# Kernel tuning notes

Measured on AMD Instinct MI355X. Metric: run time of the kernel, lower is better.

## Reference

```python
import jax, jax.numpy as jnp
import numpy as np
from jax import lax

H = 64  # hidden_size

def _lstm_layer(x, w_ih, w_hh, b_ih, b_hh):
    # x: (B, T, in). PyTorch gate order [i, f, g, o]; gates = x@W_ih^T + h@W_hh^T + b_ih + b_hh.
    B, T, _ = x.shape
    xw = jnp.einsum('bti,gi->btg', x, w_ih) + (b_ih + b_hh)  # (B, T, 4H), input projection hoisted out of scan

    def step(carry, xw_t):
        h, c = carry
        gates = xw_t + h @ w_hh.T                     # (B, 4H)
        i, f, g, o = jnp.split(gates, 4, axis=-1)
        i = jax.nn.sigmoid(i)
        f = jax.nn.sigmoid(f)
        g = jnp.tanh(g)
        o = jax.nn.sigmoid(o)
        c = f * c + i * g
        h = o * jnp.tanh(c)
        return (h, c), h

    h0 = jnp.zeros((B, H), dtype=x.dtype)
    c0 = jnp.zeros((B, H), dtype=x.dtype)
    (h_n, _), hs = lax.scan(step, (h0, c0), jnp.swapaxes(xw, 0, 1))  # hs: (T, B, H)
    return jnp.swapaxes(hs, 0, 1), h_n


def setup_inputs() -> dict:
    key = jax.random.key(0)
    ks = jax.random.split(key, 12)
    s = 1.0 / np.sqrt(H)  # PyTorch LSTM init scale
    return {
        'x':     jax.random.normal(ks[0], (2048, 512, 4), dtype=jnp.float32),
        'w_ih0': jax.random.uniform(ks[1], (4 * H, 4), jnp.float32, -s, s),
        'w_hh0': jax.random.uniform(ks[2], (4 * H, H), jnp.float32, -s, s),
        'b_ih0': jax.random.uniform(ks[3], (4 * H,), jnp.float32, -s, s),
        'b_hh0': jax.random.uniform(ks[4], (4 * H,), jnp.float32, -s, s),
        'w_ih1': jax.random.uniform(ks[5], (4 * H, H), jnp.float32, -s, s),
        'w_hh1': jax.random.uniform(ks[6], (4 * H, H), jnp.float32, -s, s),
        'b_ih1': jax.random.uniform(ks[7], (4 * H,), jnp.float32, -s, s),
        'b_hh1': jax.random.uniform(ks[8], (4 * H,), jnp.float32, -s, s),
        'fc_w':  jax.random.uniform(ks[9], (H, H), jnp.float32, -s, s),
        'fc_b':  jax.random.uniform(ks[10], (H,), jnp.float32, -s, s),
    }


def reference(x, w_ih0, w_hh0, b_ih0, b_hh0, w_ih1, w_hh1, b_ih1, b_hh1, fc_w, fc_b):
    # 2-layer LSTM (eval mode: inter-layer dropout inactive), take last layer's final hidden,
    # then Linear + tanh.
    h1_seq, _ = _lstm_layer(x, w_ih0, w_hh0, b_ih0, b_hh0)
    _, h_n = _lstm_layer(h1_seq, w_ih1, w_hh1, b_ih1, b_hh1)
    return jnp.tanh(h_n @ fc_w.T + fc_b)
```

## Files before the change

kernel.cpp:

```cpp
#include <hip/hip_runtime.h>


#define HID 64
#define TSTEPS 512
#define MB 8
#define BLK 256
#define HSTR 88
#define LOG2E  1.4426950408889634f
#define LOG2E2 2.8853900817779268f

typedef _Float16 f16;
typedef _Float16 half8 __attribute__((ext_vector_type(8)));
typedef _Float16 half4 __attribute__((ext_vector_type(4)));
typedef float f32x4 __attribute__((ext_vector_type(4)));

__device__ __forceinline__ float tanh2(float y) {
    return fmaf(2.0f, __builtin_amdgcn_rcpf(1.0f + __builtin_amdgcn_exp2f(-y)), -1.0f);
}

__global__ __launch_bounds__(BLK, 1) void lstm_mfma(
    const float* __restrict__ x,
    const float* __restrict__ w_ih0,
    const float* __restrict__ w_hh0,
    const float* __restrict__ b_ih0,
    const float* __restrict__ b_hh0,
    const float* __restrict__ w_ih1,
    const float* __restrict__ w_hh1,
    const float* __restrict__ b_ih1,
    const float* __restrict__ b_hh1,
    const float* __restrict__ fc_w,
    const float* __restrict__ fc_b,
    float* __restrict__ out)
{
    __shared__ f16 xs[TSTEPS * MB * 4];
    __shared__ f16 h0s[4][MB * HSTR];
    __shared__ f16 h1s[2][MB * HSTR];

    const int tid  = threadIdx.x;
    const int wl   = tid >> 6;
    const int l    = tid & 63;
    const int quad = l >> 4;
    const int l15  = l & 15;
    const int b0   = blockIdx.x * MB;

    const int RM = (l15 < 8) ? l15 : ((l15 & 4) | ((l15 + 2) & 3));

    for (int it = tid; it < MB * TSTEPS; it += BLK) {
        const int m = it >> 9;
        const int t = it & 511;
        const float4 v = *((const float4*)x + (size_t)(b0 + m) * TSTEPS + t);
        *(half4*)(xs + (t * MB + m) * 4) =
            (half4){ (f16)v.x, (f16)v.y, (f16)v.z, (f16)v.w };
    }
    for (int it = tid; it < MB * HSTR; it += BLK) {
        h0s[0][it] = (f16)0.f; h0s[1][it] = (f16)0.f;
        h0s[2][it] = (f16)0.f; h0s[3][it] = (f16)0.f;
        h1s[0][it] = (f16)0.f; h1s[1][it] = (f16)0.f;
    }

    half8 B0[4][3];
    half8 B1[4][4];
    f32x4 bias0[4], bias1[4];
    const half8 Z = { (f16)0.f,(f16)0.f,(f16)0.f,(f16)0.f,
                      (f16)0.f,(f16)0.f,(f16)0.f,(f16)0.f };
    #pragma unroll
    for (int ti = 0; ti < 4; ++ti) {
        const int n = (wl + 4 * ti) * 16 + l15;
        const float sc = (ti == 2) ? LOG2E2 : LOG2E;
        {
            const float bval = (b_ih0[n] + b_hh0[n]) * sc;
            half8 pz = Z;
            if (quad == 0) {
                const float4 v = *(const float4*)(w_ih0 + n * 4);
                pz[0] = (f16)(v.x * sc); pz[1] = (f16)(v.y * sc);
                pz[2] = (f16)(v.z * sc); pz[3] = (f16)(v.w * sc);
            }
            B0[ti][0] = pz;
            #pragma unroll
            for (int ks = 0; ks < 2; ++ks) {
                const int ko = ks * 32 + quad * 8;
                const float4 a = *(const float4*)(w_hh0 + n * HID + ko);
                const float4 b = *(const float4*)(w_hh0 + n * HID + ko + 4);
                B0[ti][1 + ks] = (half8){
                    (f16)(a.x*sc),(f16)(a.y*sc),(f16)(a.z*sc),(f16)(a.w*sc),
                    (f16)(b.x*sc),(f16)(b.y*sc),(f16)(b.z*sc),(f16)(b.w*sc) };
            }
            bias0[ti] = (f32x4){ bval, bval, bval, bval };
        }
        {
            const float bval = (b_ih1[n] + b_hh1[n]) * sc;
            #pragma unroll
            for (int ks = 0; ks < 2; ++ks) {
                const int ko = ks * 32 + quad * 8;
                const float4 a = *(const float4*)(w_ih1 + n * HID + ko);
                const float4 b = *(const float4*)(w_ih1 + n * HID + ko + 4);
                B1[ti][ks] = (half8){
                    (f16)(a.x*sc),(f16)(a.y*sc),(f16)(a.z*sc),(f16)(a.w*sc),
                    (f16)(b.x*sc),(f16)(b.y*sc),(f16)(b.z*sc),(f16)(b.w*sc) };
                const float4 c = *(const float4*)(w_hh1 + n * HID + ko);
                const float4 d = *(const float4*)(w_hh1 + n * HID + ko + 4);
                B1[ti][2 + ks] = (half8){
                    (f16)(c.x*sc),(f16)(c.y*sc),(f16)(c.z*sc),(f16)(c.w*sc),
                    (f16)(d.x*sc),(f16)(d.y*sc),(f16)(d.z*sc),(f16)(d.w*sc) };
            }
            bias1[ti] = (f32x4){ bval, bval, bval, bval };
        }
    }

    const int  mrow = (quad & 1) * 4 + (quad & 2);
    const int  uu   = wl * 16 + l15;
    const int  hb   = RM * HSTR + quad * 8;
    float c00 = 0.f, c01 = 0.f;
    float c10 = 0.f, c11 = 0.f;
    f32x4 g0[4], g1[4];

    auto load_x = [&](int r) -> half4 {
        return *(const half4*)(xs + (r * MB + RM) * 4);
    };
    auto l0_mfma = [&](half4 xv, half8 A1, half8 A2) {
        half8 ax = Z;
        if (quad == 0) { ax[0]=xv[0]; ax[1]=xv[1]; ax[2]=xv[2]; ax[3]=xv[3]; }
        #pragma unroll
        for (int ti = 0; ti < 4; ++ti) {
            f32x4 acc;
            acc    = __builtin_amdgcn_mfma_f32_16x16x32_f16(ax, B0[ti][0], bias0[ti], 0, 0, 0);
            acc    = __builtin_amdgcn_mfma_f32_16x16x32_f16(A1, B0[ti][1], acc, 0, 0, 0);
            g0[ti] = __builtin_amdgcn_mfma_f32_16x16x32_f16(A2, B0[ti][2], acc, 0, 0, 0);
        }
    };
    auto l1_mfma = [&](half8 A1, half8 A2, half8 A3, half8 A4) {
        #pragma unroll
        for (int ti = 0; ti < 4; ++ti) {
            f32x4 acc;
            acc    = __builtin_amdgcn_mfma_f32_16x16x32_f16(A1, B1[ti][0], bias1[ti], 0, 0, 0);
            acc    = __builtin_amdgcn_mfma_f32_16x16x32_f16(A2, B1[ti][1], acc, 0, 0, 0);
            acc    = __builtin_amdgcn_mfma_f32_16x16x32_f16(A3, B1[ti][2], acc, 0, 0, 0);
            g1[ti] = __builtin_amdgcn_mfma_f32_16x16x32_f16(A4, B1[ti][3], acc, 0, 0, 0);
        }
    };
    auto act_store = [&](const f32x4* gg, f16* dst, float& ca, float& cb) {
        #pragma unroll
        for (int j = 0; j < 2; ++j) {
            const float ei = __builtin_amdgcn_exp2f(-gg[0][j]);
            const float ef = __builtin_amdgcn_exp2f(-gg[1][j]);
            const float eg = __builtin_amdgcn_exp2f(-gg[2][j]);
            const float eo = __builtin_amdgcn_exp2f(-gg[3][j]);
            float& c = j ? cb : ca;
            const float af = 1.0f + ef;
            const float P  = (1.0f + ei) * (1.0f + eg);
            const float N  = fmaf(c * P, 1.0f, (1.0f - eg) * af);
            c = N * __builtin_amdgcn_rcpf(P * af);
            const float ym = fminf(-LOG2E2 * c, 126.0f);
            const float ec = __builtin_amdgcn_exp2f(ym);
            const float r2 = __builtin_amdgcn_rcpf((1.0f + eo) * (1.0f + ec));
            dst[(mrow + j) * HSTR + uu] = (f16)((1.0f - ec) * r2);
        }
    };

    __syncthreads();

    half4 xv = load_x(0);

    #pragma unroll 1
    for (int r = 0; r < TSTEPS; ++r) {
        const f16* h0rd = h0s[(r + 3) & 3];
        const half8 A1 = *(const half8*)(h0rd + hb);
        const half8 A2 = *(const half8*)(h0rd + hb + 32);
        if (r >= 2) act_store(g1, h1s[r & 1], c10, c11);
        l0_mfma(xv, A1, A2);
        __syncthreads();
        const f16* h1rd = h1s[r & 1];
        const half8 A3 = *(const half8*)(h1rd + hb);
        const half8 A4 = *(const half8*)(h1rd + hb + 32);
        act_store(g0, h0s[r & 3], c00, c01);
        l1_mfma(A1, A2, A3, A4);
        xv = load_x((r + 1) & 511);
        __syncthreads();
    }

    act_store(g1, h1s[0], c10, c11);
    __syncthreads();
    {
        const f16* h0rd = h0s[3];
        const half8 A1 = *(const half8*)(h0rd + hb);
        const half8 A2 = *(const half8*)(h0rd + hb + 32);
        const half8 A3 = *(const half8*)(h1s[0] + hb);
        const half8 A4 = *(const half8*)(h1s[0] + hb + 32);
        l1_mfma(A1, A2, A3, A4);
        act_store(g1, h1s[1], c10, c11);
    }
    __syncthreads();

    for (int it = tid; it < MB * HID; it += BLK) {
        const int v = it & 63;
        const int m = it >> 6;
        float a = fc_b[v];
        const f16* hp = h1s[1] + m * HSTR;
        const float4* wp = (const float4*)(fc_w + v * HID);
        #pragma unroll
        for (int kk = 0; kk < HID / 4; ++kk) {
            const float4 wv = wp[kk];
            a += (float)hp[kk * 4 + 0] * wv.x + (float)hp[kk * 4 + 1] * wv.y
               + (float)hp[kk * 4 + 2] * wv.z + (float)hp[kk * 4 + 3] * wv.w;
        }
        out[(size_t)(b0 + m) * HID + v] = tanh2(a * LOG2E2);
    }
}

extern "C" void kernel_launch(void* const* d_in, const int* in_sizes, int n_in,
                              void* d_out, int out_size, void* d_ws, size_t ws_size,
                              hipStream_t stream) {
    const float* x     = (const float*)d_in[0];
    const float* w_ih0 = (const float*)d_in[1];
    const float* w_hh0 = (const float*)d_in[2];
    const float* b_ih0 = (const float*)d_in[3];
    const float* b_hh0 = (const float*)d_in[4];
    const float* w_ih1 = (const float*)d_in[5];
    const float* w_hh1 = (const float*)d_in[6];
    const float* b_ih1 = (const float*)d_in[7];
    const float* b_hh1 = (const float*)d_in[8];
    const float* fc_w  = (const float*)d_in[9];
    const float* fc_b  = (const float*)d_in[10];
    float* out = (float*)d_out;

    const int B = in_sizes[0] / (TSTEPS * 4);
    lstm_mfma<<<dim3(B / MB), dim3(BLK), 0, stream>>>(
        x, w_ih0, w_hh0, b_ih0, b_hh0, w_ih1, w_hh1, b_ih1, b_hh1, fc_w, fc_b, out);
}
```

Before: 368.1 us.

## Interleave gate activations with MFMAs via sched_group_barrier and share reciprocals

Restructures the LSTM cell activation so the two rows share a single reciprocal for the cell update and another for the output, computed as one rcp of a product. It also adds sched_group_barrier hints to interleave MFMA instructions with VALU activation work inside each phase. Both aim to shorten the serial per-step critical path. The shared reciprocal risks overflow in the product of denominators, which is why the exp clamp drops to 60, and forced scheduling may raise register pressure.

Result: no change. 370.9 us (+0.7%).

```diff
diff --git a/kernel.cpp b/kernel.cpp
--- a/kernel.cpp
+++ b/kernel.cpp
@@ -8,6 +8,7 @@
 #define HSTR 88
 #define LOG2E  1.4426950408889634f
 #define LOG2E2 2.8853900817779268f
+#define SGB __builtin_amdgcn_sched_group_barrier
 
 typedef _Float16 f16;
 typedef _Float16 half8 __attribute__((ext_vector_type(8)));
@@ -139,21 +140,36 @@
         }
     };
     auto act_store = [&](const f32x4* gg, f16* dst, float& ca, float& cb) {
-        #pragma unroll
-        for (int j = 0; j < 2; ++j) {
-            const float ei = __builtin_amdgcn_exp2f(-gg[0][j]);
-            const float ef = __builtin_amdgcn_exp2f(-gg[1][j]);
-            const float eg = __builtin_amdgcn_exp2f(-gg[2][j]);
-            const float eo = __builtin_amdgcn_exp2f(-gg[3][j]);
-            float& c = j ? cb : ca;
-            const float af = 1.0f + ef;
-            const float P  = (1.0f + ei) * (1.0f + eg);
-            const float N  = fmaf(c * P, 1.0f, (1.0f - eg) * af);
-            c = N * __builtin_amdgcn_rcpf(P * af);
-            const float ym = fminf(-LOG2E2 * c, 126.0f);
-            const float ec = __builtin_amdgcn_exp2f(ym);
-            const float r2 = __builtin_amdgcn_rcpf((1.0f + eo) * (1.0f + ec));
-            dst[(mrow + j) * HSTR + uu] = (f16)((1.0f - ec) * r2);
+        float e0[4], e1[4];
+        #pragma unroll
+        for (int t = 0; t < 4; ++t) {
+            e0[t] = __builtin_amdgcn_exp2f(-gg[t][0]);
+            e1[t] = __builtin_amdgcn_exp2f(-gg[t][1]);
+        }
+        const float af0 = 1.0f + e0[1],            af1 = 1.0f + e1[1];
+        const float P0  = (1.0f + e0[0]) * (1.0f + e0[2]);
+        const float P1  = (1.0f + e1[0]) * (1.0f + e1[2]);
+        const float N0  = fmaf(ca, P0, (1.0f - e0[2]) * af0);
+        const float N1  = fmaf(cb, P1, (1.0f - e1[2]) * af1);
+        const float D0  = P0 * af0,                D1  = P1 * af1;
+        const float rD  = __builtin_amdgcn_rcpf(D0 * D1);
+        ca = N0 * (rD * D1);
+        cb = N1 * (rD * D0);
+        const float ec0 = __builtin_amdgcn_exp2f(fminf(-LOG2E2 * ca, 60.0f));
+        const float ec1 = __builtin_amdgcn_exp2f(fminf(-LOG2E2 * cb, 60.0f));
+        const float E0  = (1.0f + e0[3]) * (1.0f + ec0);
+        const float E1  = (1.0f + e1[3]) * (1.0f + ec1);
+        const float rE  = __builtin_amdgcn_rcpf(E0 * E1);
+        dst[(mrow + 0) * HSTR + uu] = (f16)((1.0f - ec0) * (rE * E1));
+        dst[(mrow + 1) * HSTR + uu] = (f16)((1.0f - ec1) * (rE * E0));
+    };
+    auto sgb_phase = [&](int nmfma) {
+        SGB(0x100, 2, 0);
+        SGB(0x002, 8, 0);
+        #pragma unroll
+        for (int i = 0; i < 16; ++i) {
+            if (i < 12) { SGB(0x008, 1, 0); SGB(0x002, 3, 0); }
+            else if (nmfma == 16) { SGB(0x008, 1, 0); SGB(0x002, 2, 0); }
         }
     };
 
@@ -168,6 +184,7 @@
         const half8 A2 = *(const half8*)(h0rd + hb + 32);
         if (r >= 2) act_store(g1, h1s[r & 1], c10, c11);
         l0_mfma(xv, A1, A2);
+        sgb_phase(12);
         __syncthreads();
         const f16* h1rd = h1s[r & 1];
         const half8 A3 = *(const half8*)(h1rd + hb);
@@ -175,6 +192,7 @@
         act_store(g0, h0s[r & 3], c00, c01);
         l1_mfma(A1, A2, A3, A4);
         xv = load_x((r + 1) & 511);
+        sgb_phase(16);
         __syncthreads();
     }
 
```
